# Optimization experiments

Measured on AMD Instinct MI355X. Metric: run time of the kernel, lower is better.

The kernel has to match this reference:

```python
import jax, jax.numpy as jnp
import numpy as np

TAU = 2.0        # spikingjelly LIFNode default tau
VTH = 1.0        # v_threshold
ALPHA = 2.0      # ATan surrogate alpha
NUM_HEADS = 8
N_WIN = 8
TOPK = 4


@jax.custom_vjp
def atan_heaviside(x):
    # spike = H(v - v_th), with ATan surrogate gradient
    return (x >= 0.0).astype(x.dtype)

def _ah_fwd(x):
    return atan_heaviside(x), x

def _ah_bwd(x, g):
    half_pi_alpha = np.float32(np.pi / 2.0 * ALPHA)
    return (g * (ALPHA / 2.0) / (1.0 + (half_pi_alpha * x) ** 2),)

atan_heaviside.defvjp(_ah_fwd, _ah_bwd)


def lif(x):
    """Multi-step LIF over leading time dim. decay_input=True, v_reset=0, detach_reset."""
    def step(v, xt):
        v = v + (xt - v) / TAU                      # charge
        s = atan_heaviside(v - VTH)                 # fire
        v = v * (1.0 - jax.lax.stop_gradient(s))    # hard reset (detached)
        return v, s
    _, spikes = jax.lax.scan(step, jnp.zeros_like(x[0]), x)
    return spikes


def setup_inputs() -> dict:
    key = jax.random.key(0)
    k1, k2, k3, k4, k5 = jax.random.split(key, 5)
    T, B, L, C = 4, 4, 1024, 256
    x = jax.random.normal(k1, (T, B, L, C), dtype=jnp.float32)
    w_qkv = jax.random.normal(k2, (C, 3 * C), dtype=jnp.float32) * (C ** -0.5)
    b_qkv = jax.random.normal(k3, (3 * C,), dtype=jnp.float32) * 0.02
    w_proj = jax.random.normal(k4, (C, C), dtype=jnp.float32) * (C ** -0.5)
    b_proj = jax.random.normal(k5, (C,), dtype=jnp.float32) * 0.02
    return {"x": x, "w_qkv": w_qkv, "b_qkv": b_qkv, "w_proj": w_proj, "b_proj": b_proj}


def reference(x, w_qkv, b_qkv, w_proj, b_proj):
    T, B, L, C = x.shape
    hd = C // NUM_HEADS
    win = L // N_WIN
    scale = hd ** -0.5

    # --- region-level routing (on raw input summed over time) ---
    xs = x.sum(axis=0).reshape(B, N_WIN, win, C)
    region = xs.sum(axis=2)                                  # [B, n_win, C]
    attn_r = jnp.einsum('bnc,bmc->bnm', region, region) * (C ** -0.5)
    _, idx = jax.lax.top_k(attn_r, TOPK)                     # [B, n_win, topk] int32

    # --- qkv + LIF spiking ---
    qkv = x @ w_qkv + b_qkv                                  # [T,B,L,3C]
    q, k, v = jnp.split(qkv, 3, axis=-1)
    q, k, v = lif(q), lif(k), lif(v)
    q = q.reshape(T, B, N_WIN, win, NUM_HEADS, hd)
    k = k.reshape(T, B, N_WIN, win, NUM_HEADS, hd)
    v = v.reshape(T, B, N_WIN, win, NUM_HEADS, hd)

    # --- gather routed KV windows (vectorized; topk-major concat like torch.cat) ---
    b_idx = jnp.arange(B)[:, None, None]                     # [B,1,1]
    k_g = k[:, b_idx, idx].reshape(T, B, N_WIN, TOPK * win, NUM_HEADS, hd)
    v_g = v[:, b_idx, idx].reshape(T, B, N_WIN, TOPK * win, NUM_HEADS, hd)

    # --- windowed attention over gathered keys ---
    attn = jnp.einsum('tbnqhd,tbnkhd->tbnhqk', q, k_g) * scale
    attn = jax.nn.softmax(attn, axis=-1)
    out = jnp.einsum('tbnhqk,tbnkhd->tbnqhd', attn, v_g).reshape(T, B, L, C)

    out = lif(out @ w_proj + b_proj)
    return out
```

## Files before the change

### kernel.cpp

```cpp
#include <hip/hip_runtime.h>
#include <cstdint>
#include <cstddef>

#define TT 4
#define BB 4
#define LL 1024
#define CC 256
#define HH 8
#define HD 32
#define NWIN 8
#define WIN 128
#define TOPKN 4
#define C3 768

__global__ __launch_bounds__(64) void region_kernel(const float* __restrict__ x,
                                                    float* __restrict__ region) {
    int bn = blockIdx.x;
    int b = bn >> 3, n = bn & 7;
    int c = blockIdx.y * 64 + threadIdx.x;
    float tot = 0.0f;
    for (int r = 0; r < WIN; ++r) {
        int l = n * WIN + r;
        float s = 0.0f;
        for (int t = 0; t < TT; ++t) {
            s += x[(((size_t)t * BB + b) * LL + l) * CC + c];
        }
        tot += s;
    }
    region[(size_t)bn * CC + c] = tot;
}

__global__ __launch_bounds__(64) void route_kernel(const float* __restrict__ region,
                                                   int* __restrict__ idx) {
    int b = blockIdx.x;
    __shared__ float reg[NWIN][CC];
    __shared__ float attn_r[NWIN][NWIN];
    int tid = threadIdx.x;
    for (int e = tid; e < NWIN * CC; e += 64)
        reg[e >> 8][e & 255] = region[(size_t)b * NWIN * CC + e];
    __syncthreads();
    int n = tid >> 3, m = tid & 7;
    float s = 0.0f;
    for (int c = 0; c < CC; ++c) s += reg[n][c] * reg[m][c];
    attn_r[n][m] = s * 0.0625f;
    __syncthreads();
    if (tid < NWIN) {
        float vals[NWIN];
        for (int m2 = 0; m2 < NWIN; ++m2) vals[m2] = attn_r[tid][m2];
        for (int kk = 0; kk < TOPKN; ++kk) {
            int bi = 0; float bv = vals[0];
            for (int m2 = 1; m2 < NWIN; ++m2) {
                if (vals[m2] > bv) { bv = vals[m2]; bi = m2; }
            }
            idx[(b * NWIN + tid) * TOPKN + kk] = bi;
            vals[bi] = -INFINITY;
        }
    }
}

__global__ __launch_bounds__(256, 3) void gemm_bias128(const float* __restrict__ A,
                                                       const float* __restrict__ W,
                                                       const float* __restrict__ bias,
                                                       float* __restrict__ C,
                                                       int M, int N, int K) {
    const int BM = 128, BN = 128, BK = 16, TM = 8;
    __shared__ float As[BK][BM + 4];
    __shared__ float Bs[BK][136];
    int tid = threadIdx.x;
    int tx = tid & 15, ty = tid >> 4;
    int bm = blockIdx.x * BM, bn = blockIdx.y * BN;
    float acc[TM][8] = {};
    for (int k0 = 0; k0 < K; k0 += BK) {
#pragma unroll
        for (int it = 0; it < 2; ++it) {
            int i = it * 256 + tid;
            int row = i >> 2, kc = (i & 3) * 4;
            float4 v = *(const float4*)(A + (size_t)(bm + row) * K + k0 + kc);
            As[kc + 0][row] = v.x; As[kc + 1][row] = v.y;
            As[kc + 2][row] = v.z; As[kc + 3][row] = v.w;
        }
#pragma unroll
        for (int it = 0; it < 2; ++it) {
            int i = it * 256 + tid;
            int kr = i >> 5, nc = (i & 31) * 4;
            float4 v = *(const float4*)(W + (size_t)(k0 + kr) * N + bn + nc);
            *(float4*)&Bs[kr][nc] = v;
        }
        __syncthreads();
#pragma unroll
        for (int kk = 0; kk < BK; ++kk) {
            float a[TM], bb[8];
            const float4* ap = (const float4*)&As[kk][ty * TM];
            float4 a0 = ap[0], a1 = ap[1];
            a[0]=a0.x; a[1]=a0.y; a[2]=a0.z; a[3]=a0.w;
            a[4]=a1.x; a[5]=a1.y; a[6]=a1.z; a[7]=a1.w;
            float4 b0 = *(const float4*)&Bs[kk][tx * 4];
            float4 b1 = *(const float4*)&Bs[kk][64 + tx * 4];
            bb[0]=b0.x; bb[1]=b0.y; bb[2]=b0.z; bb[3]=b0.w;
            bb[4]=b1.x; bb[5]=b1.y; bb[6]=b1.z; bb[7]=b1.w;
#pragma unroll
            for (int i = 0; i < TM; ++i)
#pragma unroll
                for (int j = 0; j < 8; ++j)
                    acc[i][j] = fmaf(a[i], bb[j], acc[i][j]);
        }
        __syncthreads();
    }
#pragma unroll
    for (int i = 0; i < TM; ++i) {
        int row = bm + ty * TM + i;
        int col0 = bn + tx * 4;
        int col1 = bn + 64 + tx * 4;
        float4 o0 = make_float4(acc[i][0] + bias[col0 + 0], acc[i][1] + bias[col0 + 1],
                                acc[i][2] + bias[col0 + 2], acc[i][3] + bias[col0 + 3]);
        float4 o1 = make_float4(acc[i][4] + bias[col1 + 0], acc[i][5] + bias[col1 + 1],
                                acc[i][6] + bias[col1 + 2], acc[i][7] + bias[col1 + 3]);
        *(float4*)&C[(size_t)row * N + col0] = o0;
        *(float4*)&C[(size_t)row * N + col1] = o1;
    }
}

__global__ __launch_bounds__(256, 4) void gemm_bias64(const float* __restrict__ A,
                                                      const float* __restrict__ W,
                                                      const float* __restrict__ bias,
                                                      float* __restrict__ C,
                                                      int M, int N, int K) {
    const int BM = 64, BN = 64, BK = 16;
    __shared__ float As[BK][BM + 4];
    __shared__ float Bs[BK][72];
    int tid = threadIdx.x;
    int tx = tid & 15, ty = tid >> 4;
    int bm = blockIdx.x * BM, bn = blockIdx.y * BN;
    float acc[4][4] = {};
    for (int k0 = 0; k0 < K; k0 += BK) {
        {
            int row = tid >> 2, kc = (tid & 3) * 4;
            float4 v = *(const float4*)(A + (size_t)(bm + row) * K + k0 + kc);
            As[kc + 0][row] = v.x; As[kc + 1][row] = v.y;
            As[kc + 2][row] = v.z; As[kc + 3][row] = v.w;
        }
        {
            int kr = tid >> 4, nc = (tid & 15) * 4;
            float4 v = *(const float4*)(W + (size_t)(k0 + kr) * N + bn + nc);
            *(float4*)&Bs[kr][nc] = v;
        }
        __syncthreads();
#pragma unroll
        for (int kk = 0; kk < BK; ++kk) {
            float4 av = *(const float4*)&As[kk][ty * 4];
            float4 bv = *(const float4*)&Bs[kk][tx * 4];
            float a[4] = {av.x, av.y, av.z, av.w};
            float bb[4] = {bv.x, bv.y, bv.z, bv.w};
#pragma unroll
            for (int i = 0; i < 4; ++i)
#pragma unroll
                for (int j = 0; j < 4; ++j)
                    acc[i][j] = fmaf(a[i], bb[j], acc[i][j]);
        }
        __syncthreads();
    }
#pragma unroll
    for (int i = 0; i < 4; ++i) {
        int row = bm + ty * 4 + i;
        int col = bn + tx * 4;
        float4 o = make_float4(acc[i][0] + bias[col + 0], acc[i][1] + bias[col + 1],
                               acc[i][2] + bias[col + 2], acc[i][3] + bias[col + 3]);
        *(float4*)&C[(size_t)row * N + col] = o;
    }
}

__global__ __launch_bounds__(256) void lif_kernel(const float* src, float* dst, size_t stride) {
    size_t i = ((size_t)blockIdx.x * blockDim.x + threadIdx.x) * 4;
    float v[4] = {0.f, 0.f, 0.f, 0.f};
    for (int t = 0; t < TT; ++t) {
        float4 xv4 = *(const float4*)(src + (size_t)t * stride + i);
        float xv[4] = {xv4.x, xv4.y, xv4.z, xv4.w};
        float sp[4];
#pragma unroll
        for (int j = 0; j < 4; ++j) {
            v[j] = v[j] + (xv[j] - v[j]) * 0.5f;
            bool fire = (v[j] >= 1.0f);
            sp[j] = fire ? 1.0f : 0.0f;
            v[j] = fire ? 0.0f : v[j];
        }
        *(float4*)(dst + (size_t)t * stride + i) = make_float4(sp[0], sp[1], sp[2], sp[3]);
    }
}

__global__ __launch_bounds__(192) void lif_pack_kernel(float* __restrict__ qkv,
                                                       uint32_t* __restrict__ pk) {
    int row = blockIdx.x;
    int tid = threadIdx.x;
    int c = tid * 4;
    int wid = tid >> 6;
    int lane = tid & 63;
    const size_t stride = (size_t)BB * LL * C3;
    float* base = qkv + (size_t)row * C3 + c;

    float v[4] = {0.f, 0.f, 0.f, 0.f};
    for (int t = 0; t < TT; ++t) {
        float4 xv4 = *(const float4*)(base + (size_t)t * stride);
        float xv[4] = {xv4.x, xv4.y, xv4.z, xv4.w};
        bool fire[4];
        float sp[4];
#pragma unroll
        for (int j = 0; j < 4; ++j) {
            v[j] = v[j] + (xv[j] - v[j]) * 0.5f;
            fire[j] = (v[j] >= 1.0f);
            sp[j] = fire[j] ? 1.0f : 0.0f;
            v[j] = fire[j] ? 0.0f : v[j];
        }
        if (c >= 512)
            *(float4*)(base + (size_t)t * stride) = make_float4(sp[0], sp[1], sp[2], sp[3]);
        unsigned long long B0 = __ballot(fire[0]);
        unsigned long long B1 = __ballot(fire[1]);
        unsigned long long B2 = __ballot(fire[2]);
        unsigned long long B3 = __ballot(fire[3]);
        if (lane < 8 && wid < 2) {
            uint32_t word = ((uint32_t)(B0 >> (8 * lane)) & 0xFFu)
                          | (((uint32_t)(B1 >> (8 * lane)) & 0xFFu) << 8)
                          | (((uint32_t)(B2 >> (8 * lane)) & 0xFFu) << 16)
                          | (((uint32_t)(B3 >> (8 * lane)) & 0xFFu) << 24);
            pk[((size_t)t * BB * LL + row) * 16 + wid * 8 + lane] = word;
        }
    }
}

__global__ __launch_bounds__(128, 2) void attn_pv(const float* __restrict__ spk,
                                                  const uint32_t* __restrict__ pk,
                                                  const int* __restrict__ idxws,
                                                  float* __restrict__ out) {
    int bid = blockIdx.x;
    int hp = bid & 3, n = (bid >> 2) & 7, b = (bid >> 5) & 3, t = bid >> 7;
    __shared__ __align__(16) float Vlds[2][64][64];
    __shared__ float ptab[33][256];
    __shared__ __align__(16) uint32_t kbs[2 * 512];
    int tid = threadIdx.x;
    int qg = tid & 15, dh = (tid >> 4) & 3, h = tid >> 6;
    int lbase = (t * BB + b) * LL;

    const int* ip = idxws + (b * NWIN + n) * TOPKN;
    int s0r = ip[0], s1r = ip[1], s2r = ip[2], s3r = ip[3];

#pragma unroll 8
    for (int e = tid; e < 1024; e += 128) {
        int hh = e >> 9, kk = e & 511;
        int w = kk >> 7;
        int sw = (w == 0) ? s0r : (w == 1) ? s1r : (w == 2) ? s2r : s3r;
        int row = sw * WIN + (kk & 127);
        kbs[e] = pk[(size_t)(lbase + row) * 16 + 8 + hp * 2 + hh];
    }
    uint32_t qw[8];
#pragma unroll
    for (int j = 0; j < 8; ++j)
        qw[j] = pk[(size_t)(lbase + n * WIN + qg + 16 * j) * 16 + hp * 2 + h];

    const float* vsrc = spk + (size_t)lbase * C3 + 512 + hp * 64
                        + (size_t)(tid >> 4) * C3 + (tid & 15) * 4;
    int wvoff = (tid >> 6) * 1024;

#define STAGE_HALF(hw_)                                                              \
    do {                                                                             \
        int hw = (hw_);                                                              \
        int ww = hw >> 1;                                                            \
        int sw = (ww == 0) ? s0r : (ww == 1) ? s1r : (ww == 2) ? s2r : s3r;          \
        const float* src = vsrc + (size_t)(sw * WIN + (hw & 1) * 64) * C3;           \
        char* lb = (char*)(&Vlds[hw & 1][0][0]) + wvoff;                             \
        _Pragma("unroll")                                                            \
        for (int it = 0; it < 8; ++it) {                                             \
            __builtin_amdgcn_global_load_lds(                                        \
                (const __attribute__((address_space(1))) void*)(src + (size_t)it * 8 * C3), \
                (__attribute__((address_space(3))) void*)(lb + it * 2048), 16, 0, 0);\
        }                                                                            \
    } while (0)

    STAGE_HALF(0);
    STAGE_HALF(1);

    asm volatile("s_waitcnt lgkmcnt(0)" ::: "memory");
    __builtin_amdgcn_s_barrier();

    const float ALPHA_SC = 0.17677669529663687f;
    for (int u = tid; u < 256; u += 128) {
        int qq = u & 127, hu = u >> 7;
        uint32_t qwt = pk[(size_t)(lbase + n * WIN + qq) * 16 + hp * 2 + hu];
        const uint4* kb4u = (const uint4*)(kbs + hu * 512);
        int smax = 0;
#pragma unroll 8
        for (int k4 = 0; k4 < 128; ++k4) {
            uint4 w4 = kb4u[k4];
            smax = max(smax, __popc(qwt & w4.x));
            smax = max(smax, __popc(qwt & w4.y));
            smax = max(smax, __popc(qwt & w4.z));
            smax = max(smax, __popc(qwt & w4.w));
        }
        float am = __fmul_rn((float)smax, ALPHA_SC);
        for (int s = 0; s <= 32; ++s)
            ptab[s][u] = expf(__fsub_rn(__fmul_rn((float)s, ALPHA_SC), am));
        float Z = 0.0f;
#pragma unroll 4
        for (int k4 = 0; k4 < 128; ++k4) {
            uint4 w4 = kb4u[k4];
            Z += ptab[__popc(qwt & w4.x)][u];
            Z += ptab[__popc(qwt & w4.y)][u];
            Z += ptab[__popc(qwt & w4.z)][u];
            Z += ptab[__popc(qwt & w4.w)][u];
        }
        for (int s = 0; s <= 32; ++s)
            ptab[s][u] = ptab[s][u] / Z;
    }

    float acc[8][8];
#pragma unroll
    for (int j = 0; j < 8; ++j)
#pragma unroll
        for (int d = 0; d < 8; ++d) acc[j][d] = 0.0f;

    asm volatile("s_waitcnt lgkmcnt(0)" ::: "memory");
    asm volatile("s_waitcnt vmcnt(8)" ::: "memory");
    __builtin_amdgcn_s_barrier();

    const uint4* kb4h = (const uint4*)(kbs + h * 512);
    int hcol = h * 128 + qg;

#pragma unroll 1
    for (int hw = 0; hw < 8; ++hw) {
        const uint4* kw4 = kb4h + hw * 16;
        const float* vhalf = &Vlds[hw & 1][0][h * 32 + dh * 8];
#pragma unroll 2
        for (int g = 0; g < 16; ++g) {
            uint4 kw = kw4[g];
            const float* pr = vhalf + g * 256;
#pragma unroll
            for (int rr = 0; rr < 4; ++rr) {
                uint32_t krow = (rr == 0) ? kw.x : (rr == 1) ? kw.y
                              : (rr == 2) ? kw.z : kw.w;
                float P0 = ptab[__popc(qw[0] & krow)][hcol];
                float P1 = ptab[__popc(qw[1] & krow)][hcol + 16];
                float P2 = ptab[__popc(qw[2] & krow)][hcol + 32];
                float P3 = ptab[__popc(qw[3] & krow)][hcol + 48];
                float P4 = ptab[__popc(qw[4] & krow)][hcol + 64];
                float P5 = ptab[__popc(qw[5] & krow)][hcol + 80];
                float P6 = ptab[__popc(qw[6] & krow)][hcol + 96];
                float P7 = ptab[__popc(qw[7] & krow)][hcol + 112];
                const float4* vp = (const float4*)(pr + rr * 64);
                float4 v0 = vp[0], v1 = vp[1];
                float vv[8] = {v0.x, v0.y, v0.z, v0.w, v1.x, v1.y, v1.z, v1.w};
#pragma unroll
                for (int d = 0; d < 8; ++d) {
                    acc[0][d] = fmaf(P0, vv[d], acc[0][d]);
                    acc[1][d] = fmaf(P1, vv[d], acc[1][d]);
                    acc[2][d] = fmaf(P2, vv[d], acc[2][d]);
                    acc[3][d] = fmaf(P3, vv[d], acc[3][d]);
                    acc[4][d] = fmaf(P4, vv[d], acc[4][d]);
                    acc[5][d] = fmaf(P5, vv[d], acc[5][d]);
                    acc[6][d] = fmaf(P6, vv[d], acc[6][d]);
                    acc[7][d] = fmaf(P7, vv[d], acc[7][d]);
                }
            }
        }

        if (hw < 7) {
            __builtin_amdgcn_s_barrier();
            if (hw < 6) {
                STAGE_HALF(hw + 2);
                asm volatile("s_waitcnt vmcnt(8)" ::: "memory");
            } else {
                asm volatile("s_waitcnt vmcnt(0)" ::: "memory");
            }
            __builtin_amdgcn_s_barrier();
        }
    }
#undef STAGE_HALF

#pragma unroll
    for (int j = 0; j < 8; ++j) {
        size_t ob = (size_t)(lbase + n * WIN + qg + 16 * j) * CC
                    + (hp * 2 + h) * 32 + dh * 8;
        *(float4*)&out[ob]     = make_float4(acc[j][0], acc[j][1], acc[j][2], acc[j][3]);
        *(float4*)&out[ob + 4] = make_float4(acc[j][4], acc[j][5], acc[j][6], acc[j][7]);
    }
}

extern "C" void kernel_launch(void* const* d_in, const int* in_sizes, int n_in,
                              void* d_out, int out_size, void* d_ws, size_t ws_size,
                              hipStream_t stream) {
    const float* x      = (const float*)d_in[0];
    const float* w_qkv  = (const float*)d_in[1];
    const float* b_qkv  = (const float*)d_in[2];
    const float* w_proj = (const float*)d_in[3];
    const float* b_proj = (const float*)d_in[4];
    float* ws = (float*)d_ws;

    float* qkv      = ws;
    float* attn_out = ws + 12582912;
    float* proj     = ws + 16777216;
    uint32_t* pkb   = (uint32_t*)proj;
    float* region   = ws + 20971520;
    int*   idxp     = (int*)(ws + 20979712);
    float* outp     = (float*)d_out;

    region_kernel<<<dim3(BB * NWIN, 4), dim3(64), 0, stream>>>(x, region);
    route_kernel<<<dim3(BB), dim3(64), 0, stream>>>(region, idxp);
    gemm_bias128<<<dim3(128, 6), dim3(256), 0, stream>>>(x, w_qkv, b_qkv, qkv,
                                                         TT * BB * LL, C3, CC);
    lif_pack_kernel<<<dim3(BB * LL), dim3(192), 0, stream>>>(qkv, pkb);
    attn_pv<<<dim3(TT * BB * NWIN * 4), dim3(128), 0, stream>>>(qkv, pkb, idxp, attn_out);
    gemm_bias64<<<dim3(256, 4), dim3(256), 0, stream>>>(attn_out, w_proj, b_proj, proj,
                                                        TT * BB * LL, CC, CC);
    lif_kernel<<<dim3(1024), dim3(256), 0, stream>>>(proj, outp, (size_t)BB * LL * CC);
}
```

Baseline: 258.1 us.

## Bit-pack V spikes and rebuild attention PV loop on packed bits

The LIF pack kernel now emits packed bitmasks for V as well as Q and K (24 words per row) and no longer writes float V spikes back to the qkv buffer. The attention kernel loads K and V bitmasks into LDS, drops the double-buffered float V staging through global_load_lds and its barriers, and unpacks V bits in registers for the PV accumulation. It also moves to 256 threads with 4 query rows per thread instead of 8. This removes most V global traffic and the store of spikes, at the cost of extra bit-extract and convert ALU work per FMA.

```diff
diff --git a/kernel.cpp b/kernel.cpp
--- a/kernel.cpp
+++ b/kernel.cpp
@@ -12,6 +12,7 @@
 #define WIN 128
 #define TOPKN 4
 #define C3 768
+#define PKW 24
 
 __global__ __launch_bounds__(64) void region_kernel(const float* __restrict__ x,
                                                     float* __restrict__ region) {
@@ -187,7 +188,7 @@
     }
 }
 
-__global__ __launch_bounds__(192) void lif_pack_kernel(float* __restrict__ qkv,
+__global__ __launch_bounds__(192) void lif_pack_kernel(const float* __restrict__ qkv,
                                                        uint32_t* __restrict__ pk) {
     int row = blockIdx.x;
     int tid = threadIdx.x;
@@ -195,96 +196,68 @@
     int wid = tid >> 6;
     int lane = tid & 63;
     const size_t stride = (size_t)BB * LL * C3;
-    float* base = qkv + (size_t)row * C3 + c;
+    const float* base = qkv + (size_t)row * C3 + c;
 
     float v[4] = {0.f, 0.f, 0.f, 0.f};
     for (int t = 0; t < TT; ++t) {
         float4 xv4 = *(const float4*)(base + (size_t)t * stride);
         float xv[4] = {xv4.x, xv4.y, xv4.z, xv4.w};
         bool fire[4];
-        float sp[4];
 #pragma unroll
         for (int j = 0; j < 4; ++j) {
             v[j] = v[j] + (xv[j] - v[j]) * 0.5f;
             fire[j] = (v[j] >= 1.0f);
-            sp[j] = fire[j] ? 1.0f : 0.0f;
             v[j] = fire[j] ? 0.0f : v[j];
         }
-        if (c >= 512)
-            *(float4*)(base + (size_t)t * stride) = make_float4(sp[0], sp[1], sp[2], sp[3]);
         unsigned long long B0 = __ballot(fire[0]);
         unsigned long long B1 = __ballot(fire[1]);
         unsigned long long B2 = __ballot(fire[2]);
         unsigned long long B3 = __ballot(fire[3]);
-        if (lane < 8 && wid < 2) {
+        if (lane < 8) {
             uint32_t word = ((uint32_t)(B0 >> (8 * lane)) & 0xFFu)
                           | (((uint32_t)(B1 >> (8 * lane)) & 0xFFu) << 8)
                           | (((uint32_t)(B2 >> (8 * lane)) & 0xFFu) << 16)
                           | (((uint32_t)(B3 >> (8 * lane)) & 0xFFu) << 24);
-            pk[((size_t)t * BB * LL + row) * 16 + wid * 8 + lane] = word;
-        }
-    }
-}
-
-__global__ __launch_bounds__(128, 2) void attn_pv(const float* __restrict__ spk,
-                                                  const uint32_t* __restrict__ pk,
+            pk[((size_t)t * BB * LL + row) * PKW + wid * 8 + lane] = word;
+        }
+    }
+}
+
+__global__ __launch_bounds__(256, 2) void attn_pv(const uint32_t* __restrict__ pk,
                                                   const int* __restrict__ idxws,
                                                   float* __restrict__ out) {
     int bid = blockIdx.x;
     int hp = bid & 3, n = (bid >> 2) & 7, b = (bid >> 5) & 3, t = bid >> 7;
-    __shared__ __align__(16) float Vlds[2][64][64];
     __shared__ float ptab[33][256];
-    __shared__ __align__(16) uint32_t kbs[2 * 512];
-    int tid = threadIdx.x;
-    int qg = tid & 15, dh = (tid >> 4) & 3, h = tid >> 6;
+    __shared__ uint32_t kbs[2][512];
+    __shared__ uint32_t vbs[2][512];
+    int tid = threadIdx.x;
+    int qg = tid & 31, dh = (tid >> 5) & 3, h = tid >> 7;
     int lbase = (t * BB + b) * LL;
 
     const int* ip = idxws + (b * NWIN + n) * TOPKN;
     int s0r = ip[0], s1r = ip[1], s2r = ip[2], s3r = ip[3];
 
-#pragma unroll 8
-    for (int e = tid; e < 1024; e += 128) {
+#pragma unroll 4
+    for (int e = tid; e < 1024; e += 256) {
         int hh = e >> 9, kk = e & 511;
         int w = kk >> 7;
         int sw = (w == 0) ? s0r : (w == 1) ? s1r : (w == 2) ? s2r : s3r;
-        int row = sw * WIN + (kk & 127);
-        kbs[e] = pk[(size_t)(lbase + row) * 16 + 8 + hp * 2 + hh];
-    }
-    uint32_t qw[8];
-#pragma unroll
-    for (int j = 0; j < 8; ++j)
-        qw[j] = pk[(size_t)(lbase + n * WIN + qg + 16 * j) * 16 + hp * 2 + h];
-
-    const float* vsrc = spk + (size_t)lbase * C3 + 512 + hp * 64
-                        + (size_t)(tid >> 4) * C3 + (tid & 15) * 4;
-    int wvoff = (tid >> 6) * 1024;
-
-#define STAGE_HALF(hw_)                                                              \
-    do {                                                                             \
-        int hw = (hw_);                                                              \
-        int ww = hw >> 1;                                                            \
-        int sw = (ww == 0) ? s0r : (ww == 1) ? s1r : (ww == 2) ? s2r : s3r;          \
-        const float* src = vsrc + (size_t)(sw * WIN + (hw & 1) * 64) * C3;           \
-        char* lb = (char*)(&Vlds[hw & 1][0][0]) + wvoff;                             \
-        _Pragma("unroll")                                                            \
-        for (int it = 0; it < 8; ++it) {                                             \
-            __builtin_amdgcn_global_load_lds(                                        \
-                (const __attribute__((address_space(1))) void*)(src + (size_t)it * 8 * C3), \
-                (__attribute__((address_space(3))) void*)(lb + it * 2048), 16, 0, 0);\
-        }                                                                            \
-    } while (0)
-
-    STAGE_HALF(0);
-    STAGE_HALF(1);
-
-    asm volatile("s_waitcnt lgkmcnt(0)" ::: "memory");
-    __builtin_amdgcn_s_barrier();
+        size_t rowb = (size_t)(lbase + sw * WIN + (kk & 127)) * PKW + hp * 2 + hh;
+        kbs[hh][kk] = pk[rowb + 8];
+        vbs[hh][kk] = pk[rowb + 16];
+    }
+    uint32_t qw[4];
+#pragma unroll
+    for (int j = 0; j < 4; ++j)
+        qw[j] = pk[(size_t)(lbase + n * WIN + qg + 32 * j) * PKW + hp * 2 + h];
+    __syncthreads();
 
     const float ALPHA_SC = 0.17677669529663687f;
-    for (int u = tid; u < 256; u += 128) {
-        int qq = u & 127, hu = u >> 7;
-        uint32_t qwt = pk[(size_t)(lbase + n * WIN + qq) * 16 + hp * 2 + hu];
-        const uint4* kb4u = (const uint4*)(kbs + hu * 512);
+    {
+        int qq = tid & 127, hu = tid >> 7;
+        uint32_t qwt = pk[(size_t)(lbase + n * WIN + qq) * PKW + hp * 2 + hu];
+        const uint4* kb4u = (const uint4*)kbs[hu];
         int smax = 0;
 #pragma unroll 8
         for (int k4 = 0; k4 < 128; ++k4) {
@@ -296,86 +269,57 @@
         }
         float am = __fmul_rn((float)smax, ALPHA_SC);
         for (int s = 0; s <= 32; ++s)
-            ptab[s][u] = expf(__fsub_rn(__fmul_rn((float)s, ALPHA_SC), am));
+            ptab[s][tid] = expf(__fsub_rn(__fmul_rn((float)s, ALPHA_SC), am));
         float Z = 0.0f;
 #pragma unroll 4
         for (int k4 = 0; k4 < 128; ++k4) {
             uint4 w4 = kb4u[k4];
-            Z += ptab[__popc(qwt & w4.x)][u];
-            Z += ptab[__popc(qwt & w4.y)][u];
-            Z += ptab[__popc(qwt & w4.z)][u];
-            Z += ptab[__popc(qwt & w4.w)][u];
+            Z += ptab[__popc(qwt & w4.x)][tid];
+            Z += ptab[__popc(qwt & w4.y)][tid];
+            Z += ptab[__popc(qwt & w4.z)][tid];
+            Z += ptab[__popc(qwt & w4.w)][tid];
         }
         for (int s = 0; s <= 32; ++s)
-            ptab[s][u] = ptab[s][u] / Z;
-    }
-
-    float acc[8][8];
-#pragma unroll
-    for (int j = 0; j < 8; ++j)
-#pragma unroll
-        for (int d = 0; d < 8; ++d) acc[j][d] = 0.0f;
-
-    asm volatile("s_waitcnt lgkmcnt(0)" ::: "memory");
-    asm volatile("s_waitcnt vmcnt(8)" ::: "memory");
-    __builtin_amdgcn_s_barrier();
-
-    const uint4* kb4h = (const uint4*)(kbs + h * 512);
-    int hcol = h * 128 + qg;
+            ptab[s][tid] = ptab[s][tid] / Z;
+    }
+    __syncthreads();
+
+    const uint4* kb4 = (const uint4*)kbs[h];
+    const uint32_t* vbh = vbs[h];
+    int c0 = h * 128 + qg;
+    int po = 2 * dh;
+    float acc[4][8];
+#pragma unroll
+    for (int j = 0; j < 4; ++j)
+#pragma unroll
+        for (int e = 0; e < 8; ++e) acc[j][e] = 0.0f;
 
 #pragma unroll 1
-    for (int hw = 0; hw < 8; ++hw) {
-        const uint4* kw4 = kb4h + hw * 16;
-        const float* vhalf = &Vlds[hw & 1][0][h * 32 + dh * 8];
-#pragma unroll 2
-        for (int g = 0; g < 16; ++g) {
-            uint4 kw = kw4[g];
-            const float* pr = vhalf + g * 256;
-#pragma unroll
-            for (int rr = 0; rr < 4; ++rr) {
-                uint32_t krow = (rr == 0) ? kw.x : (rr == 1) ? kw.y
-                              : (rr == 2) ? kw.z : kw.w;
-                float P0 = ptab[__popc(qw[0] & krow)][hcol];
-                float P1 = ptab[__popc(qw[1] & krow)][hcol + 16];
-                float P2 = ptab[__popc(qw[2] & krow)][hcol + 32];
-                float P3 = ptab[__popc(qw[3] & krow)][hcol + 48];
-                float P4 = ptab[__popc(qw[4] & krow)][hcol + 64];
-                float P5 = ptab[__popc(qw[5] & krow)][hcol + 80];
-                float P6 = ptab[__popc(qw[6] & krow)][hcol + 96];
-                float P7 = ptab[__popc(qw[7] & krow)][hcol + 112];
-                const float4* vp = (const float4*)(pr + rr * 64);
-                float4 v0 = vp[0], v1 = vp[1];
-                float vv[8] = {v0.x, v0.y, v0.z, v0.w, v1.x, v1.y, v1.z, v1.w};
-#pragma unroll
-                for (int d = 0; d < 8; ++d) {
-                    acc[0][d] = fmaf(P0, vv[d], acc[0][d]);
-                    acc[1][d] = fmaf(P1, vv[d], acc[1][d]);
-                    acc[2][d] = fmaf(P2, vv[d], acc[2][d]);
-                    acc[3][d] = fmaf(P3, vv[d], acc[3][d]);
-                    acc[4][d] = fmaf(P4, vv[d], acc[4][d]);
-                    acc[5][d] = fmaf(P5, vv[d], acc[5][d]);
-                    acc[6][d] = fmaf(P6, vv[d], acc[6][d]);
-                    acc[7][d] = fmaf(P7, vv[d], acc[7][d]);
-                }
+    for (int g = 0; g < 128; ++g) {
+        uint4 kw = kb4[g];
+#pragma unroll
+        for (int r = 0; r < 4; ++r) {
+            uint32_t krow = (r == 0) ? kw.x : (r == 1) ? kw.y : (r == 2) ? kw.z : kw.w;
+            uint32_t sh = vbh[g * 4 + r] >> po;
+            float P0 = ptab[__popc(qw[0] & krow)][c0];
+            float P1 = ptab[__popc(qw[1] & krow)][c0 + 32];
+            float P2 = ptab[__popc(qw[2] & krow)][c0 + 64];
+            float P3 = ptab[__popc(qw[3] & krow)][c0 + 96];
+#pragma unroll
+            for (int e = 0; e < 8; ++e) {
+                const int offs = (e & 3) * 8 + (e >> 2);
+                float vf = (float)((sh >> offs) & 1u);
+                acc[0][e] = fmaf(P0, vf, acc[0][e]);
+                acc[1][e] = fmaf(P1, vf, acc[1][e]);
+                acc[2][e] = fmaf(P2, vf, acc[2][e]);
+                acc[3][e] = fmaf(P3, vf, acc[3][e]);
             }
         }
-
-        if (hw < 7) {
-            __builtin_amdgcn_s_barrier();
-            if (hw < 6) {
-                STAGE_HALF(hw + 2);
-                asm volatile("s_waitcnt vmcnt(8)" ::: "memory");
-            } else {
-                asm volatile("s_waitcnt vmcnt(0)" ::: "memory");
-            }
-            __builtin_amdgcn_s_barrier();
-        }
-    }
-#undef STAGE_HALF
-
-#pragma unroll
-    for (int j = 0; j < 8; ++j) {
-        size_t ob = (size_t)(lbase + n * WIN + qg + 16 * j) * CC
+    }
+
+#pragma unroll
+    for (int j = 0; j < 4; ++j) {
+        size_t ob = (size_t)(lbase + n * WIN + qg + 32 * j) * CC
                     + (hp * 2 + h) * 32 + dh * 8;
         *(float4*)&out[ob]     = make_float4(acc[j][0], acc[j][1], acc[j][2], acc[j][3]);
         *(float4*)&out[ob + 4] = make_float4(acc[j][4], acc[j][5], acc[j][6], acc[j][7]);
@@ -405,7 +349,7 @@
     gemm_bias128<<<dim3(128, 6), dim3(256), 0, stream>>>(x, w_qkv, b_qkv, qkv,
                                                          TT * BB * LL, C3, CC);
     lif_pack_kernel<<<dim3(BB * LL), dim3(192), 0, stream>>>(qkv, pkb);
-    attn_pv<<<dim3(TT * BB * NWIN * 4), dim3(128), 0, stream>>>(qkv, pkb, idxp, attn_out);
+    attn_pv<<<dim3(TT * BB * NWIN * 4), dim3(256), 0, stream>>>(pkb, idxp, attn_out);
     gemm_bias64<<<dim3(256, 4), dim3(256), 0, stream>>>(attn_out, w_proj, b_proj, proj,
                                                         TT * BB * LL, CC, CC);
     lif_kernel<<<dim3(1024), dim3(256), 0, stream>>>(proj, outp, (size_t)BB * LL * CC);
```

Result: slower. 268.6 us (+4.0%).
